# Kernel tuning notes

Hardware: AMD Instinct MI355X
Metric: run time of the kernel (lower is better)

The kernel has to match this reference:

```python
import jax, jax.numpy as jnp
import numpy as np

T, N, H, DIN = 128, 256, 512, 255  # inputs last dim = DIN + 1 (trailing action channel)
PACK = H + 5  # packed state: a(1), loc(1), scale(1), v(1), h(H), p(1)


def setup_inputs() -> dict:
    key = jax.random.key(0)
    ks = jax.random.split(key, 12)
    f32 = jnp.float32
    def rn(k, shape, scale):
        return jax.random.normal(k, shape, dtype=f32) * scale
    si, sh = 1.0 / np.sqrt(DIN), 1.0 / np.sqrt(H)
    return {
        "inputs": jax.random.normal(ks[0], (T, N, DIN + 1), dtype=f32),
        "hx": rn(ks[1], (1, N, PACK), 0.1),
        "eps": jax.random.normal(ks[2], (T, N, 1), dtype=f32),
        "Wih": rn(ks[3], (3 * H, DIN), si),
        "Whh": rn(ks[4], (3 * H, H), sh),
        "bih": jnp.zeros((3 * H,), f32),
        "bhh": jnp.zeros((3 * H,), f32),
        "Wa0": rn(ks[5], (H, H), sh), "ba0": jnp.zeros((H,), f32),
        "Wa1": rn(ks[6], (H, H), sh), "ba1": jnp.zeros((H,), f32),
        "Wloc": rn(ks[7], (1, H), sh), "bloc": jnp.zeros((1,), f32),
        "logstd": jnp.zeros((1,), f32),
        "Wc0": rn(ks[8], (H, H), sh), "bc0": jnp.zeros((H,), f32),
        "Wc1": rn(ks[9], (H, H), sh), "bc1": jnp.zeros((H,), f32),
        "Wv": rn(ks[10], (1, H), sh), "bv": jnp.zeros((1,), f32),
    }


def _forward(inputs, hx, eps, Wih, Whh, bih, bhh, Wa0, ba0, Wa1, ba1,
             Wloc, bloc, logstd, Wc0, bc0, Wc1, bc1, Wv, bv):
    inputs = jax.lax.stop_gradient(inputs)  # module calls inputs.detach()
    obs, actions = inputs[..., :DIN], inputs[..., DIN:]
    hx0 = hx[0]                       # [N, PACK] after squeeze_(0)
    h0 = hx0[:, 4:4 + H]              # initial GRU hidden state
    p = hx0[:, H + 4:H + 5]           # [N,1], passed through unchanged

    def step(h, x_t):
        # PyTorch GRU cell math
        gi = x_t @ Wih.T + bih        # [N, 3H]
        gh = h @ Whh.T + bhh          # [N, 3H]
        ir, iz, in_ = jnp.split(gi, 3, axis=-1)
        hr, hz, hn = jnp.split(gh, 3, axis=-1)
        r = jax.nn.sigmoid(ir + hr)
        z = jax.nn.sigmoid(iz + hz)
        n = jnp.tanh(in_ + r * hn)
        h_new = (1.0 - z) * n + z * h
        return h_new, h_new

    _, hs = jax.lax.scan(step, h0, obs)  # [T, N, H]; hn == h for 1-layer unidir GRU

    def mlp2(x, W0, b0, W1, b1):
        return jnp.tanh(jnp.tanh(x @ W0.T + b0) @ W1.T + b1)

    # heads don't feed back into the recurrence -> apply to all timesteps at once
    loc = mlp2(hs, Wa0, ba0, Wa1, ba1) @ Wloc.T + bloc        # [T, N, 1]
    scale = jnp.broadcast_to(jnp.exp(logstd), loc.shape)      # DiagGaussian scale
    v = mlp2(hs, Wc0, bc0, Wc1, bc1) @ Wv.T + bv              # [T, N, 1]

    # sample_new: replace entries of A where actions < 0 with dist.sample()
    sample = jax.lax.stop_gradient(loc + scale * eps)         # .sample() is non-differentiable
    a = jnp.where(actions < 0, sample, actions)

    p_full = jnp.broadcast_to(p, (T, N, 1))
    # pack() order follows RecurrentState fields: a, loc, scale, v, h, p
    return jnp.concatenate([a, loc, scale, v, hs, p_full], axis=-1)  # [T, N, PACK]


def reference(inputs, hx, eps, Wih, Whh, bih, bhh, Wa0, ba0, Wa1, ba1,
              Wloc, bloc, logstd, Wc0, bc0, Wc1, bc1, Wv, bv):
    packed = _forward(inputs, hx, eps, Wih, Whh, bih, bhh, Wa0, ba0, Wa1, ba1,
                      Wloc, bloc, logstd, Wc0, bc0, Wc1, bc1, Wv, bv)
    return (packed, packed[-1:])
```

## Files before the change

kernel.cpp:

```cpp
#include <hip/hip_runtime.h>

typedef unsigned short u16;
typedef unsigned long long u64;
typedef __bf16 bf16x8 __attribute__((ext_vector_type(8)));
typedef float f32x4 __attribute__((ext_vector_type(4)));

#define T_STEPS 128
#define NB 256
#define HDIM 512
#define DIN_ 255
#define PACK_ 517
#define TN 32768

__device__ __forceinline__ float b2f(u16 u) {
    union { unsigned int i; float f; } v; v.i = ((unsigned int)u) << 16; return v.f;
}
__device__ __forceinline__ u16 f2b(float f) {
    union { float f; unsigned int i; } v; v.f = f;
    unsigned int r = v.i + 0x7FFFu + ((v.i >> 16) & 1u);
    return (u16)(r >> 16);
}
__device__ __forceinline__ float sigm(float x) { return 1.f / (1.f + __expf(-x)); }
__device__ __forceinline__ float ftanh(float x) { return 2.f * sigm(2.f * x) - 1.f; }

template<int DO_TANH, int K, int MT>
__global__ __launch_bounds__(256) void gemm_bt(const u16* __restrict__ A,
                                               const u16* __restrict__ B,
                                               const float* __restrict__ bias,
                                               u16* __restrict__ C, int N) {
    __shared__ u16 lds[64 * K];
    int n0 = blockIdx.x * 64;
    int w = threadIdx.x >> 6, l = threadIdx.x & 63;
    int la = l & 15, lb = l >> 4;
    for (int idx = threadIdx.x; idx < 8 * K; idx += 256) {
        int kq = idx >> 6, row = idx & 63;
        *(bf16x8*)(lds + (size_t)idx * 8) =
            *(const bf16x8*)(B + (size_t)(n0 + row) * K + kq * 8);
    }
    __syncthreads();
    const u16* bq[4];
    #pragma unroll
    for (int c = 0; c < 4; ++c) bq[c] = lds + ((size_t)lb * 64 + 16 * c + la) * 8;

    for (int mt = 0; mt < MT; ++mt) {
        int m0 = (blockIdx.y * MT + mt) * 64;
        int mw = m0 + 16 * w;
        const u16* Ap = A + (size_t)(mw + la) * K + 8 * lb;
        f32x4 acc[4] = {};
        #pragma unroll
        for (int k0 = 0; k0 < K; k0 += 32) {
            bf16x8 a = *(const bf16x8*)(Ap + k0);
            #pragma unroll
            for (int c = 0; c < 4; ++c)
                acc[c] = __builtin_amdgcn_mfma_f32_16x16x32_bf16(
                    a, *(const bf16x8*)(bq[c] + (size_t)k0 * 64), acc[c], 0, 0, 0);
        }
        #pragma unroll
        for (int c = 0; c < 4; ++c) {
            int n = n0 + 16 * c + la;
            float bv = bias[n];
            #pragma unroll
            for (int r = 0; r < 4; ++r) {
                int m = mw + 4 * lb + r;
                float v = acc[c][r] + bv;
                if (DO_TANH) v = ftanh(v);
                C[(size_t)m * N + n] = f2b(v);
            }
        }
    }
}

__global__ __launch_bounds__(256, 1) void gru_persist(
    const u16* __restrict__ h0b, const float* __restrict__ hx,
    const u16* __restrict__ whh_b, const float* __restrict__ bhh,
    const u16* __restrict__ gi_b, float* __restrict__ out,
    u16* __restrict__ hs_b, unsigned int* __restrict__ bar) {
    extern __shared__ u16 lds[];
    const int tid = threadIdx.x;
    const int b = blockIdx.x >> 4, ksl = blockIdx.x & 15;
    const int ks = ksl * 32, m0 = b * 64;
    const int w = tid >> 6, l = tid & 63;
    const int la = l & 15, lb = l >> 4;
    const int mw = m0 + 16 * w;

    for (int idx = tid; idx < 6144; idx += 256) {
        int kq = idx / 96, row = idx - kq * 96;
        int g = row >> 5, rr = row & 31;
        *(bf16x8*)(lds + (size_t)idx * 8) =
            *(const bf16x8*)(whh_b + (size_t)(g * HDIM + ks + rr) * HDIM + kq * 8);
    }
    const u16* bq[6];
    #pragma unroll
    for (int c = 0; c < 6; ++c) {
        int lr = (c >> 1) * 32 + (c & 1) * 16 + la;
        bq[c] = lds + (size_t)(lb * 96 + lr) * 8;
    }
    float bh[3][2];
    #pragma unroll
    for (int g = 0; g < 3; ++g)
        #pragma unroll
        for (int cc = 0; cc < 2; ++cc)
            bh[g][cc] = bhh[g * HDIM + ks + 16 * cc + la];
    float hp[2][4];
    #pragma unroll
    for (int cc = 0; cc < 2; ++cc)
        #pragma unroll
        for (int r = 0; r < 4; ++r)
            hp[cc][r] = hx[(size_t)(mw + 4 * lb + r) * PACK_ + 4 + ks + 16 * cc + la];

    __syncthreads();
    unsigned int* mybar = bar + b * 64;

    for (int t = 0; t < T_STEPS; ++t) {
        const u16* gi_t = gi_b + (size_t)t * NB * 3 * HDIM;

        u16 giv[3][2][4];
        #pragma unroll
        for (int r = 0; r < 4; ++r) {
            const u16* gp = gi_t + (size_t)(mw + 4 * lb + r) * 1536 + ks + la;
            #pragma unroll
            for (int g = 0; g < 3; ++g)
                #pragma unroll
                for (int cc = 0; cc < 2; ++cc)
                    giv[g][cc][r] = gp[g * HDIM + 16 * cc];
        }

        if (t > 0) {
            if (tid == 0) {
                unsigned tgt = 16u * (unsigned)t;
                while (__hip_atomic_load(mybar, __ATOMIC_RELAXED,
                                         __HIP_MEMORY_SCOPE_AGENT) < tgt)
                    __builtin_amdgcn_s_sleep(1);
            }
            __syncthreads();
            asm volatile("" ::: "memory");
        }

        const u16* Ap = (t ? hs_b + (size_t)(t - 1) * NB * HDIM : h0b)
                        + (size_t)(mw + la) * HDIM + 8 * lb;
        bf16x8 a[16];
        #pragma unroll
        for (int kk = 0; kk < 16; ++kk) {
            union { u64 q[2]; bf16x8 v; } u;
            u.q[0] = __hip_atomic_load((const u64*)(Ap + 32 * kk),
                                       __ATOMIC_RELAXED, __HIP_MEMORY_SCOPE_AGENT);
            u.q[1] = __hip_atomic_load((const u64*)(Ap + 32 * kk + 4),
                                       __ATOMIC_RELAXED, __HIP_MEMORY_SCOPE_AGENT);
            a[kk] = u.v;
        }

        f32x4 acc[6] = {};
        #pragma unroll
        for (int kk = 0; kk < 16; ++kk) {
            #pragma unroll
            for (int c = 0; c < 6; ++c)
                acc[c] = __builtin_amdgcn_mfma_f32_16x16x32_bf16(
                    a[kk], *(const bf16x8*)(bq[c] + (size_t)kk * 3072), acc[c], 0, 0, 0);
        }

        float* out_t = out + (size_t)t * NB * PACK_;
        u16* hs_t = hs_b + (size_t)t * NB * HDIM;
        #pragma unroll
        for (int cc = 0; cc < 2; ++cc) {
            #pragma unroll
            for (int r = 0; r < 4; ++r) {
                int n = mw + 4 * lb + r;
                int k = ks + 16 * cc + la;
                float hr = acc[0 + cc][r] + bh[0][cc];
                float hz = acc[2 + cc][r] + bh[1][cc];
                float hn = acc[4 + cc][r] + bh[2][cc];
                float rr = sigm(b2f(giv[0][cc][r]) + hr);
                float zz = sigm(b2f(giv[1][cc][r]) + hz);
                float nn = ftanh(b2f(giv[2][cc][r]) + rr * hn);
                float hnew = (1.f - zz) * nn + zz * hp[cc][r];
                hp[cc][r] = hnew;
                out_t[(size_t)n * PACK_ + 4 + k] = hnew;
                float nbv = __shfl_xor(hnew, 1, 64);
                if (!(la & 1)) {
                    unsigned pack = (unsigned)f2b(hnew) | ((unsigned)f2b(nbv) << 16);
                    __hip_atomic_store(
                        (unsigned*)(hs_t + (size_t)n * HDIM + ks + 16 * cc + (la & ~1)),
                        pack, __ATOMIC_RELAXED, __HIP_MEMORY_SCOPE_AGENT);
                }
            }
        }

        if (t < T_STEPS - 1) {
            __syncthreads();
            if (tid == 0)
                __hip_atomic_fetch_add(mybar, 1u, __ATOMIC_RELAXED,
                                       __HIP_MEMORY_SCOPE_AGENT);
        }
    }
}

__global__ __launch_bounds__(256) void head_dot(const u16* __restrict__ X,
                                                const u16* __restrict__ W,
                                                const float* __restrict__ b,
                                                float* __restrict__ out, int off) {
    int wid = (int)((blockIdx.x * blockDim.x + threadIdx.x) >> 6);
    int l = threadIdx.x & 63;
    if (wid >= TN) return;
    bf16x8 xv = *(const bf16x8*)(X + (size_t)wid * HDIM + 8 * l);
    bf16x8 wv = *(const bf16x8*)(W + 8 * l);
    float s = 0.f;
    #pragma unroll
    for (int j = 0; j < 8; ++j) s += (float)xv[j] * (float)wv[j];
    #pragma unroll
    for (int d = 32; d; d >>= 1) s += __shfl_down(s, d, 64);
    if (l == 0) out[(size_t)wid * PACK_ + off] = s + b[0];
}

__global__ void prep_w(const float* __restrict__ Wih, const float* __restrict__ Whh,
                       const float* __restrict__ Wa0, const float* __restrict__ Wa1,
                       const float* __restrict__ Wloc, const float* __restrict__ Wc0,
                       const float* __restrict__ Wc1, const float* __restrict__ Wv,
                       const float* __restrict__ hx,
                       u16* Wih_b, u16* Whh_b, u16* Wa0_b, u16* Wa1_b,
                       u16* Wloc_b, u16* Wc0_b, u16* Wc1_b, u16* Wv_b,
                       float* h0f, u16* h0b) {
    int i = blockIdx.x * 256 + threadIdx.x;
    if (i < 1536 * 256) { int r = i >> 8, c = i & 255;
        Wih_b[i] = (c < DIN_) ? f2b(Wih[r * DIN_ + c]) : (u16)0; return; }
    i -= 1536 * 256;
    if (i < 1536 * 512) { Whh_b[i] = f2b(Whh[i]); return; } i -= 1536 * 512;
    if (i < 512 * 512) { Wa0_b[i] = f2b(Wa0[i]); return; } i -= 512 * 512;
    if (i < 512 * 512) { Wa1_b[i] = f2b(Wa1[i]); return; } i -= 512 * 512;
    if (i < 512 * 512) { Wc0_b[i] = f2b(Wc0[i]); return; } i -= 512 * 512;
    if (i < 512 * 512) { Wc1_b[i] = f2b(Wc1[i]); return; } i -= 512 * 512;
    if (i < 512) { Wloc_b[i] = f2b(Wloc[i]); return; } i -= 512;
    if (i < 512) { Wv_b[i] = f2b(Wv[i]); return; } i -= 512;
    if (i < NB * HDIM) { int n = i >> 9, k = i & 511;
        float v = hx[n * PACK_ + 4 + k]; h0f[i] = v; h0b[i] = f2b(v); return; }
}

__global__ void prep_obs(const float* __restrict__ in, u16* __restrict__ obs) {
    int idx = blockIdx.x * 256 + threadIdx.x;
    if (idx >= TN * 32) return;
    int m = idx >> 5, j = idx & 31;
    const float* src = in + (size_t)m * 256 + 8 * j;
    union { u16 s[8]; uint4 u; } t;
    #pragma unroll
    for (int q = 0; q < 8; ++q) t.s[q] = f2b(src[q]);
    if (j == 31) t.s[7] = 0;
    *(uint4*)(obs + (size_t)m * 256 + 8 * j) = t.u;
}

__global__ void finalize_out(const float* __restrict__ in, const float* __restrict__ eps,
                             const float* __restrict__ hx, const float* __restrict__ logstd,
                             float* __restrict__ out) {
    int m = blockIdx.x * 256 + threadIdx.x;
    if (m >= TN) return;
    int n = m & (NB - 1);
    float scale = __expf(logstd[0]);
    float loc = out[(size_t)m * PACK_ + 1];
    float act = in[(size_t)m * 256 + DIN_];
    float a = (act < 0.f) ? (loc + scale * eps[m]) : act;
    out[(size_t)m * PACK_ + 0] = a;
    out[(size_t)m * PACK_ + 2] = scale;
    out[(size_t)m * PACK_ + PACK_ - 1] = hx[n * PACK_ + PACK_ - 1];
}

__global__ void tail_copy(float* __restrict__ out) {
    int i = blockIdx.x * 256 + threadIdx.x;
    if (i >= NB * PACK_) return;
    out[(size_t)T_STEPS * NB * PACK_ + i] = out[(size_t)(T_STEPS - 1) * NB * PACK_ + i];
}

extern "C" void kernel_launch(void* const* d_in, const int* in_sizes, int n_in,
                              void* d_out, int out_size, void* d_ws, size_t ws_size,
                              hipStream_t stream) {
    const float* inputs = (const float*)d_in[0];
    const float* hx     = (const float*)d_in[1];
    const float* eps    = (const float*)d_in[2];
    const float* Wih    = (const float*)d_in[3];
    const float* Whh    = (const float*)d_in[4];
    const float* bih    = (const float*)d_in[5];
    const float* bhh    = (const float*)d_in[6];
    const float* Wa0    = (const float*)d_in[7];
    const float* ba0    = (const float*)d_in[8];
    const float* Wa1    = (const float*)d_in[9];
    const float* ba1    = (const float*)d_in[10];
    const float* Wloc   = (const float*)d_in[11];
    const float* bloc   = (const float*)d_in[12];
    const float* logstd = (const float*)d_in[13];
    const float* Wc0    = (const float*)d_in[14];
    const float* bc0    = (const float*)d_in[15];
    const float* Wc1    = (const float*)d_in[16];
    const float* bc1    = (const float*)d_in[17];
    const float* Wv     = (const float*)d_in[18];
    const float* bv     = (const float*)d_in[19];
    float* out = (float*)d_out;
    char* ws = (char*)d_ws;

    const size_t o_gi   = 0;
    const size_t o_buf0 = 0;
    const size_t o_buf1 = 33554432;
    const size_t o_hs   = 100663296;
    const size_t o_obs  = o_hs + 33554432;
    const size_t o_whh  = o_obs + 16777216;
    const size_t o_wih  = o_whh + 1572864;
    const size_t o_wa0  = o_wih + 786432;
    const size_t o_wa1  = o_wa0 + 524288;
    const size_t o_wc0  = o_wa1 + 524288;
    const size_t o_wc1  = o_wc0 + 524288;
    const size_t o_wloc = o_wc1 + 524288;
    const size_t o_wv   = o_wloc + 1024;
    const size_t o_h0f  = o_wv + 1024;
    const size_t o_h0b  = o_h0f + 524288;
    const size_t o_bar  = o_h0b + 262144;
    const size_t NEED   = o_bar + 4096;
    if (ws_size < NEED) return;

    u16*   gi_b   = (u16*)(ws + o_gi);
    u16*   buf0   = (u16*)(ws + o_buf0);
    u16*   buf1   = (u16*)(ws + o_buf1);
    u16*   hs_b   = (u16*)(ws + o_hs);
    u16*   obs_b  = (u16*)(ws + o_obs);
    u16*   whh_b  = (u16*)(ws + o_whh);
    u16*   wih_b  = (u16*)(ws + o_wih);
    u16*   wa0_b  = (u16*)(ws + o_wa0);
    u16*   wa1_b  = (u16*)(ws + o_wa1);
    u16*   wc0_b  = (u16*)(ws + o_wc0);
    u16*   wc1_b  = (u16*)(ws + o_wc1);
    u16*   wloc_b = (u16*)(ws + o_wloc);
    u16*   wv_b   = (u16*)(ws + o_wv);
    float* h0f    = (float*)(ws + o_h0f);
    u16*   h0b    = (u16*)(ws + o_h0b);
    unsigned int* bar = (unsigned int*)(ws + o_bar);

    static bool attr_set = false;
    if (!attr_set) {
        hipFuncSetAttribute((const void*)gru_persist,
                            hipFuncAttributeMaxDynamicSharedMemorySize, 98304);
        attr_set = true;
    }

    hipMemsetAsync(bar, 0, 4096, stream);

    prep_w<<<9220, 256, 0, stream>>>(Wih, Whh, Wa0, Wa1, Wloc, Wc0, Wc1, Wv, hx,
                                     wih_b, whh_b, wa0_b, wa1_b, wloc_b, wc0_b, wc1_b, wv_b,
                                     h0f, h0b);
    prep_obs<<<4096, 256, 0, stream>>>(inputs, obs_b);

    gemm_bt<0, 256, 8><<<dim3(24, 64), 256, 0, stream>>>(obs_b, wih_b, bih, gi_b, 1536);

    gru_persist<<<64, 256, 98304, stream>>>(h0b, hx, whh_b, bhh, gi_b, out, hs_b, bar);

    gemm_bt<1, 512, 8><<<dim3(8, 64), 256, 0, stream>>>(hs_b, wa0_b, ba0, buf0, 512);
    gemm_bt<1, 512, 8><<<dim3(8, 64), 256, 0, stream>>>(buf0, wa1_b, ba1, buf1, 512);
    head_dot<<<8192, 256, 0, stream>>>(buf1, wloc_b, bloc, out, 1);
    gemm_bt<1, 512, 8><<<dim3(8, 64), 256, 0, stream>>>(hs_b, wc0_b, bc0, buf0, 512);
    gemm_bt<1, 512, 8><<<dim3(8, 64), 256, 0, stream>>>(buf0, wc1_b, bc1, buf1, 512);
    head_dot<<<8192, 256, 0, stream>>>(buf1, wv_b, bv, out, 3);

    finalize_out<<<128, 256, 0, stream>>>(inputs, eps, hx, logstd, out);
    tail_copy<<<518, 256, 0, stream>>>(out);
}
```

Baseline: 1.418 ms.

## Use per-wave barrier signaling and cache-bypass vector loads/stores in persistent GRU

Replaces the block-wide syncthreads plus single-thread spin with per-wave spinning and per-wave counter increments, so the target becomes 64 per step. The hidden-state exchange now uses 16-byte cache-bypassing (sc0 sc1) loads and stores instead of 8-byte relaxed atomics. New h values are staged in an extra LDS buffer so each lane writes one full 16-byte row chunk. The MFMA chain is split so the first half can start after half of the loads arrive, and the fp32 output store is moved after the barrier signal to take it off the critical path. The risk is that correctness now depends on inline asm cache-control semantics and vmcnt ordering instead of atomic memory ordering.

Measured after the change: 1.452 ms. 2.4% more time.

```diff
diff --git a/kernel.cpp b/kernel.cpp
--- a/kernel.cpp
+++ b/kernel.cpp
@@ -22,6 +22,20 @@
 }
 __device__ __forceinline__ float sigm(float x) { return 1.f / (1.f + __expf(-x)); }
 __device__ __forceinline__ float ftanh(float x) { return 2.f * sigm(2.f * x) - 1.f; }
+
+__device__ __forceinline__ bf16x8 ldx4_bypass(const u16* p) {
+    f32x4 t;
+    asm volatile("global_load_dwordx4 %0, %1, off sc0 sc1"
+                 : "=v"(t) : "v"(p) : "memory");
+    union { f32x4 f; bf16x8 b; } u; u.f = t; return u.b;
+}
+__device__ __forceinline__ void stx4_bypass(u16* p, bf16x8 v) {
+    union { bf16x8 b; f32x4 f; } u; u.b = v;
+    asm volatile("global_store_dwordx4 %0, %1, off sc0 sc1"
+                 :: "v"(p), "v"(u.f) : "memory");
+}
+#define WAIT_VMCNT(N) asm volatile("s_waitcnt vmcnt(" #N ")" ::: "memory")
+#define WAIT_LGKM0    asm volatile("s_waitcnt lgkmcnt(0)" ::: "memory")
 
 template<int DO_TANH, int K, int MT>
 __global__ __launch_bounds__(256) void gemm_bt(const u16* __restrict__ A,
@@ -108,6 +122,8 @@
         for (int r = 0; r < 4; ++r)
             hp[cc][r] = hx[(size_t)(mw + 4 * lb + r) * PACK_ + 4 + ks + 16 * cc + la];
 
+    u16* packbuf = lds + 49152 + w * 512;
+
     __syncthreads();
     unsigned int* mybar = bar + b * 64;
 
@@ -126,46 +142,43 @@
         }
 
         if (t > 0) {
-            if (tid == 0) {
-                unsigned tgt = 16u * (unsigned)t;
-                while (__hip_atomic_load(mybar, __ATOMIC_RELAXED,
-                                         __HIP_MEMORY_SCOPE_AGENT) < tgt)
-                    __builtin_amdgcn_s_sleep(1);
-            }
-            __syncthreads();
-            asm volatile("" ::: "memory");
+            unsigned tgt = 64u * (unsigned)t;
+            while (__hip_atomic_load(mybar, __ATOMIC_RELAXED,
+                                     __HIP_MEMORY_SCOPE_AGENT) < tgt)
+                __builtin_amdgcn_s_sleep(1);
         }
 
         const u16* Ap = (t ? hs_b + (size_t)(t - 1) * NB * HDIM : h0b)
                         + (size_t)(mw + la) * HDIM + 8 * lb;
         bf16x8 a[16];
         #pragma unroll
-        for (int kk = 0; kk < 16; ++kk) {
-            union { u64 q[2]; bf16x8 v; } u;
-            u.q[0] = __hip_atomic_load((const u64*)(Ap + 32 * kk),
-                                       __ATOMIC_RELAXED, __HIP_MEMORY_SCOPE_AGENT);
-            u.q[1] = __hip_atomic_load((const u64*)(Ap + 32 * kk + 4),
-                                       __ATOMIC_RELAXED, __HIP_MEMORY_SCOPE_AGENT);
-            a[kk] = u.v;
-        }
+        for (int kk = 0; kk < 16; ++kk) a[kk] = ldx4_bypass(Ap + 32 * kk);
 
         f32x4 acc[6] = {};
-        #pragma unroll
-        for (int kk = 0; kk < 16; ++kk) {
+        WAIT_VMCNT(8);
+        __builtin_amdgcn_sched_barrier(0);
+        #pragma unroll
+        for (int kk = 0; kk < 8; ++kk) {
             #pragma unroll
             for (int c = 0; c < 6; ++c)
                 acc[c] = __builtin_amdgcn_mfma_f32_16x16x32_bf16(
                     a[kk], *(const bf16x8*)(bq[c] + (size_t)kk * 3072), acc[c], 0, 0, 0);
         }
-
-        float* out_t = out + (size_t)t * NB * PACK_;
-        u16* hs_t = hs_b + (size_t)t * NB * HDIM;
+        WAIT_VMCNT(0);
+        __builtin_amdgcn_sched_barrier(0);
+        #pragma unroll
+        for (int kk = 8; kk < 16; ++kk) {
+            #pragma unroll
+            for (int c = 0; c < 6; ++c)
+                acc[c] = __builtin_amdgcn_mfma_f32_16x16x32_bf16(
+                    a[kk], *(const bf16x8*)(bq[c] + (size_t)kk * 3072), acc[c], 0, 0, 0);
+        }
+
+        float hnewv[2][4];
         #pragma unroll
         for (int cc = 0; cc < 2; ++cc) {
             #pragma unroll
             for (int r = 0; r < 4; ++r) {
-                int n = mw + 4 * lb + r;
-                int k = ks + 16 * cc + la;
                 float hr = acc[0 + cc][r] + bh[0][cc];
                 float hz = acc[2 + cc][r] + bh[1][cc];
                 float hn = acc[4 + cc][r] + bh[2][cc];
@@ -174,23 +187,40 @@
                 float nn = ftanh(b2f(giv[2][cc][r]) + rr * hn);
                 float hnew = (1.f - zz) * nn + zz * hp[cc][r];
                 hp[cc][r] = hnew;
-                out_t[(size_t)n * PACK_ + 4 + k] = hnew;
-                float nbv = __shfl_xor(hnew, 1, 64);
+                hnewv[cc][r] = hnew;
+            }
+        }
+
+        #pragma unroll
+        for (int cc = 0; cc < 2; ++cc) {
+            #pragma unroll
+            for (int r = 0; r < 4; ++r) {
+                float nbv = __shfl_xor(hnewv[cc][r], 1, 64);
                 if (!(la & 1)) {
-                    unsigned pack = (unsigned)f2b(hnew) | ((unsigned)f2b(nbv) << 16);
-                    __hip_atomic_store(
-                        (unsigned*)(hs_t + (size_t)n * HDIM + ks + 16 * cc + (la & ~1)),
-                        pack, __ATOMIC_RELAXED, __HIP_MEMORY_SCOPE_AGENT);
+                    unsigned pk = (unsigned)f2b(hnewv[cc][r]) |
+                                  ((unsigned)f2b(nbv) << 16);
+                    *(unsigned*)(packbuf + (4 * lb + r) * 32 + 16 * cc + la) = pk;
                 }
             }
         }
-
-        if (t < T_STEPS - 1) {
-            __syncthreads();
-            if (tid == 0)
-                __hip_atomic_fetch_add(mybar, 1u, __ATOMIC_RELAXED,
-                                       __HIP_MEMORY_SCOPE_AGENT);
-        }
+        WAIT_LGKM0;
+        __builtin_amdgcn_sched_barrier(0);
+        bf16x8 hv = *(const bf16x8*)(packbuf + (l >> 2) * 32 + 8 * (l & 3));
+        u16* hs_t = hs_b + (size_t)t * NB * HDIM;
+        stx4_bypass(hs_t + (size_t)(m0 + 16 * w + (l >> 2)) * HDIM + ks + 8 * (l & 3), hv);
+
+        WAIT_VMCNT(0);
+        if (t < T_STEPS - 1 && l == 0)
+            __hip_atomic_fetch_add(mybar, 1u, __ATOMIC_RELAXED,
+                                   __HIP_MEMORY_SCOPE_AGENT);
+
+        float* out_t = out + (size_t)t * NB * PACK_;
+        #pragma unroll
+        for (int cc = 0; cc < 2; ++cc)
+            #pragma unroll
+            for (int r = 0; r < 4; ++r)
+                out_t[(size_t)(mw + 4 * lb + r) * PACK_ + 4 + ks + 16 * cc + la] =
+                    hnewv[cc][r];
     }
 }
 
@@ -332,7 +362,7 @@
     static bool attr_set = false;
     if (!attr_set) {
         hipFuncSetAttribute((const void*)gru_persist,
-                            hipFuncAttributeMaxDynamicSharedMemorySize, 98304);
+                            hipFuncAttributeMaxDynamicSharedMemorySize, 102400);
         attr_set = true;
     }
 
@@ -345,7 +375,7 @@
 
     gemm_bt<0, 256, 8><<<dim3(24, 64), 256, 0, stream>>>(obs_b, wih_b, bih, gi_b, 1536);
 
-    gru_persist<<<64, 256, 98304, stream>>>(h0b, hx, whh_b, bhh, gi_b, out, hs_b, bar);
+    gru_persist<<<64, 256, 102400, stream>>>(h0b, hx, whh_b, bhh, gi_b, out, hs_b, bar);
 
     gemm_bt<1, 512, 8><<<dim3(8, 64), 256, 0, stream>>>(hs_b, wa0_b, ba0, buf0, 512);
     gemm_bt<1, 512, 8><<<dim3(8, 64), 256, 0, stream>>>(buf0, wa1_b, ba1, buf1, 512);
```
